# Performance work log

Hardware: AMD Instinct MI355X
Metric: run time of the kernel (lower is better)

The kernel has to match this reference:

```python
import jax, jax.numpy as jnp
import numpy as np


def _conv(x, w, stride, dil):
    # VALID conv in NCHW / OIHW layout with rhs (kernel) dilation
    return jax.lax.conv_general_dilated(
        x, w, window_strides=stride, padding='VALID', rhs_dilation=dil,
        dimension_numbers=('NCHW', 'OIHW', 'NCHW'))


def setup_inputs() -> dict:
    key = jax.random.key(0)
    k1, k2, k3 = jax.random.split(key, 3)
    B, Cin, H, W = 8, 64, 256, 256  # W even => columns_mod2 == 0
    Cout = 128
    inp = jax.random.normal(k1, (B, Cin, H, W), dtype=jnp.float32)
    # kaiming-normal-style init as in the torch module
    fan0 = Cin * 3 * 1
    kernel0 = jax.random.normal(k2, (Cout, Cin, 3, 1), dtype=jnp.float32) * np.float32(np.sqrt(2.0 / fan0))
    fan1 = Cin * 2 * 2
    kernel1 = jax.random.normal(k3, (Cout, Cin, 2, 2), dtype=jnp.float32) * np.float32(np.sqrt(2.0 / fan1))
    bias = jnp.full((Cout,), 0.01, dtype=jnp.float32)
    return {'input': inp, 'kernel0': kernel0, 'kernel1': kernel1, 'bias': bias}


def reference(input, kernel0, kernel1, bias):
    # hexagdly conv2d, size=1, stride=1, even number of columns (columns_mod2 = 0)
    x = input
    # kernel0: vertical 3x1 stencil over all columns; bias added once here
    even_all = _conv(jnp.pad(x, ((0, 0), (0, 0), (1, 1), (0, 0))), kernel0, (1, 1), (1, 1))
    even_all = even_all + bias[None, :, None, None]
    # kernel1: 2x2 stencil with horizontal dilation 2, stride 2 in width,
    # with column-parity-dependent vertical offset (hex grid)
    # odd columns: ZeroPad2d(left=1, right=0, top=1, bottom=0)
    ooc = _conv(jnp.pad(x, ((0, 0), (0, 0), (1, 0), (1, 0))), kernel1, (1, 2), (1, 2))
    # even columns: ZeroPad2d(left=0, right=1, top=0, bottom=1)
    oec = _conv(jnp.pad(x, ((0, 0), (0, 0), (0, 1), (0, 1))), kernel1, (1, 2), (1, 2))
    # interleave columns: out[..., 2k] = ooc[..., k], out[..., 2k+1] = oec[..., k]
    B, C, H, Wh = ooc.shape
    inter = jnp.stack([ooc, oec], axis=-1).reshape(B, C, H, 2 * Wh)
    return even_all + inter
```

## Files before the change

kernel.cpp:

```cpp
#include <hip/hip_runtime.h>
#include <hip/hip_bf16.h>


#define CIN  64
#define COUT 128
#define HH   256
#define WW   256
#define TH   8
#define TW   32
#define XR   10
#define XC   34

typedef __attribute__((ext_vector_type(8))) short short8;
typedef __attribute__((ext_vector_type(4))) float f32x4;

static __device__ __forceinline__ unsigned short f2bf(float v) {
    __hip_bfloat16 h = __float2bfloat16(v);
    return __builtin_bit_cast(unsigned short, h);
}

typedef __attribute__((address_space(1))) const unsigned int asg_u32;
typedef __attribute__((address_space(3))) unsigned int asl_u32;
static __device__ __forceinline__ void gl2lds16(const void* g, void* l) {
    __builtin_amdgcn_global_load_lds((asg_u32*)g, (asl_u32*)l, 16, 0, 0);
}

#define XS_BYTES   (XR * XC * CIN * 2)
#define WTB_OFF    XS_BYTES
#define SMEM_BYTES (XS_BYTES + 2 * COUT * CIN * 2)
#define OT_STRIDE  33
#define WTAP       (COUT * CIN)

__global__ __launch_bounds__(512)
void prep_weights(const float* __restrict__ k0, const float* __restrict__ k1,
                  unsigned short* __restrict__ wsw)
{
    const int idx = blockIdx.x * 512 + threadIdx.x;
    if (idx >= 7 * COUT * 8) return;
    const int t   = idx >> 10;
    const int co  = (idx >> 3) & 127;
    const int ci0 = (idx & 7) * 8;
    short8 wv;
    #pragma unroll
    for (int j = 0; j < 8; ++j) {
        const int ci = ci0 + j;
        float v = (t < 3) ? k0[(co * CIN + ci) * 3 + t]
                          : k1[(co * CIN + ci) * 4 + (t - 3)];
        wv[j] = (short)f2bf(v);
    }
    const int e = (co * CIN + ci0) ^ ((co & 7) * 8);
    *(short8*)&wsw[t * WTAP + e] = wv;
}

__global__ __launch_bounds__(512, 4)
void hexconv_mfma(const float* __restrict__ x,
                  const unsigned short* __restrict__ wsw,
                  const float* __restrict__ bias,
                  float* __restrict__ out)
{
    __shared__ alignas(16) char smem[SMEM_BYTES];
    __shared__ float bias_lds[COUT];
    unsigned short* xs  = (unsigned short*)smem;
    unsigned short* wtb = (unsigned short*)(smem + WTB_OFF);
    float*          ot  = (float*)smem;

    const int tid  = threadIdx.x;
    const int lane = tid & 63;
    const int wid  = tid >> 6;

    const int wg = (blockIdx.x & 7) * 256 + (blockIdx.x >> 3);
    const int bx = wg & 7;
    const int by = (wg >> 3) & 31;
    const int b  = wg >> 8;

    const int h0 = by * TH;
    const int w0 = bx * TW;

    auto stage_tap = [&](int t, int buf) {
        const unsigned short* s0 = wsw + t * WTAP + wid * 1024;
        unsigned short* d0 = wtb + buf * WTAP + wid * 1024;
        gl2lds16(s0 + lane * 8, d0);
        gl2lds16(s0 + 512 + lane * 8, d0 + 512);
    };

    stage_tap(0, 0);

    if (tid < COUT) bias_lds[tid] = bias[tid];

    {
        const float* xb = x + (size_t)b * CIN * HH * WW;
        const int c = tid & 31;
        const int g = tid >> 5;
        for (int p = g; p < XR * 32; p += 16) {
            const int cip = p & 31;
            const int row = p >> 5;
            const int ci  = cip * 2;
            const int gh  = h0 - 1 + row;
            float v0 = 0.f, v1 = 0.f;
            if ((unsigned)gh < HH) {
                const float* pr = xb + ((size_t)ci * HH + gh) * WW + w0 + c;
                v0 = pr[0];
                v1 = pr[HH * WW];
            }
            unsigned int pk = (unsigned int)f2bf(v0) | ((unsigned int)f2bf(v1) << 16);
            const int col = c + 1;
            const int e = ((row * XC + col) * CIN + ci) ^ ((col & 7) * 8);
            *(unsigned int*)&xs[e] = pk;
        }
        for (int i = tid; i < 2 * XR * CIN; i += 512) {
            const int side = (i >= XR * CIN) ? 1 : 0;
            const int rem  = i - side * XR * CIN;
            const int row  = rem >> 6;
            const int ci   = rem & 63;
            const int col  = side ? (XC - 1) : 0;
            const int gh   = h0 - 1 + row;
            const int gw   = side ? (w0 + TW) : (w0 - 1);
            float v = 0.f;
            if ((unsigned)gh < HH && (unsigned)gw < WW)
                v = xb[((size_t)ci * HH + gh) * WW + gw];
            const int e = ((row * XC + col) * CIN + ci) ^ ((col & 7) * 8);
            xs[e] = f2bf(v);
        }
    }

    __syncthreads();

    const int wm   = wid & 1;
    const int wn   = wid >> 1;
    const int c15  = lane & 15;
    const int q8   = (lane >> 4) * 8;
    const int par  = lane & 1;

    const int aBase = (wm * 64 + c15) * CIN + q8;
    const int swzA  = (c15 & 7) * 8;

    f32x4 acc[4][4];
    #pragma unroll
    for (int mi = 0; mi < 4; ++mi)
        #pragma unroll
        for (int ni = 0; ni < 4; ++ni)
            acc[mi][ni] = (f32x4)0.0f;

    for (int tap = 0; tap < 7; ++tap) {
        if (tap < 6) stage_tap(tap + 1, (tap + 1) & 1);

        const unsigned short* wc = wtb + (tap & 1) * WTAP;

        int R0, P, C0;
        if (tap < 3) { R0 = tap; P = 0; C0 = 1; }
        else { R0 = (tap - 3) >> 1; P = 1; C0 = ((tap - 3) & 1) * 2; }
        const int colb  = c15 + C0;
        const int swzB  = (colb & 7) * 8;
        const int bBase = ((wn * 2 + R0 + P * par) * XC + colb) * CIN + q8;

        #pragma unroll
        for (int ci0 = 0; ci0 < CIN; ci0 += 32) {
            short8 af[4];
            #pragma unroll
            for (int mi = 0; mi < 4; ++mi)
                af[mi] = *(const short8*)&wc[(aBase + mi * 16 * CIN + ci0) ^ swzA];
            #pragma unroll
            for (int ni = 0; ni < 4; ++ni) {
                const int hr = ni >> 1, chalf = ni & 1;
                const int e = (bBase + hr * (XC * CIN) + chalf * (16 * CIN) + ci0) ^ swzB;
                short8 bf = *(const short8*)&xs[e];
                #pragma unroll
                for (int mi = 0; mi < 4; ++mi)
                    acc[mi][ni] = __builtin_amdgcn_mfma_f32_16x16x32_bf16(
                        af[mi], bf, acc[mi][ni], 0, 0, 0);
            }
        }
        __syncthreads();
    }

    #pragma unroll
    for (int p = 0; p < 2; ++p) {
        if (wm == p) {
            #pragma unroll
            for (int mi = 0; mi < 4; ++mi) {
                #pragma unroll
                for (int ni = 0; ni < 4; ++ni) {
                    const int hh   = wn * 2 + (ni >> 1);
                    const int wloc = (ni & 1) * 16 + c15;
                    #pragma unroll
                    for (int r = 0; r < 4; ++r) {
                        const int col = mi * 16 + (lane >> 4) * 4 + r;
                        ot[(col * TH + hh) * OT_STRIDE + wloc] =
                            acc[mi][ni][r] + bias_lds[p * 64 + col];
                    }
                }
            }
        }
        __syncthreads();
        #pragma unroll
        for (int it = 0; it < 8; ++it) {
            const int col = it * 8 + (tid >> 6);
            const int hh  = (tid >> 3) & 7;
            const int w4  = (tid & 7) * 4;
            const float* src = &ot[(col * TH + hh) * OT_STRIDE + w4];
            f32x4 v = { src[0], src[1], src[2], src[3] };
            __builtin_nontemporal_store(v,
                (f32x4*)&out[(((size_t)b * COUT + p * 64 + col) * HH + h0 + hh) * WW + w0 + w4]);
        }
        if (p == 0) __syncthreads();
    }
}

extern "C" void kernel_launch(void* const* d_in, const int* in_sizes, int n_in,
                              void* d_out, int out_size, void* d_ws, size_t ws_size,
                              hipStream_t stream) {
    const float* x    = (const float*)d_in[0];
    const float* k0   = (const float*)d_in[1];
    const float* k1   = (const float*)d_in[2];
    const float* bias = (const float*)d_in[3];
    float* out        = (float*)d_out;
    unsigned short* wsw = (unsigned short*)d_ws;

    prep_weights<<<dim3(14, 1, 1), 512, 0, stream>>>(k0, k1, wsw);
    hexconv_mfma<<<dim3(2048, 1, 1), 512, 0, stream>>>(x, wsw, bias, out);
}
```

Baseline: 113.7 us.

## Vectorize input tile loads and replace syncthreads with fine-grained waitcnt barriers

The input tile staging now loads four consecutive floats per thread with 128-bit global loads instead of scalar loads, which cuts the number of load instructions. The tap loop is fully unrolled, and each __syncthreads is replaced by explicit s_waitcnt vmcnt/lgkmcnt plus raw s_barrier. This lets the next tap's weight prefetch stay in flight while the current tap computes, instead of draining every outstanding memory operation at each barrier. The vmcnt(2) counting assumes that only the two prefetch loads are outstanding. If the compiler reorders or adds loads, this could cause a subtle race.

Result: faster. 98.41 us (-13.4%).

```diff
diff --git a/kernel.cpp b/kernel.cpp
--- a/kernel.cpp
+++ b/kernel.cpp
@@ -89,23 +89,27 @@
 
     {
         const float* xb = x + (size_t)b * CIN * HH * WW;
-        const int c = tid & 31;
-        const int g = tid >> 5;
-        for (int p = g; p < XR * 32; p += 16) {
-            const int cip = p & 31;
-            const int row = p >> 5;
-            const int ci  = cip * 2;
+        const int cg = tid & 7;
+        const int u0 = tid >> 3;
+        #pragma unroll
+        for (int it = 0; it < 5; ++it) {
+            const int u   = u0 + it * 64;
+            const int row = u >> 5;
+            const int ci  = (u & 31) * 2;
             const int gh  = h0 - 1 + row;
-            float v0 = 0.f, v1 = 0.f;
+            f32x4 a = (f32x4)0.0f, c = (f32x4)0.0f;
             if ((unsigned)gh < HH) {
-                const float* pr = xb + ((size_t)ci * HH + gh) * WW + w0 + c;
-                v0 = pr[0];
-                v1 = pr[HH * WW];
-            }
-            unsigned int pk = (unsigned int)f2bf(v0) | ((unsigned int)f2bf(v1) << 16);
-            const int col = c + 1;
-            const int e = ((row * XC + col) * CIN + ci) ^ ((col & 7) * 8);
-            *(unsigned int*)&xs[e] = pk;
+                const float* pb = xb + ((size_t)ci * HH + gh) * WW + w0 + 4 * cg;
+                a = *(const f32x4*)pb;
+                c = *(const f32x4*)(pb + HH * WW);
+            }
+            #pragma unroll
+            for (int k = 0; k < 4; ++k) {
+                const int col = 4 * cg + 1 + k;
+                unsigned int pk = (unsigned int)f2bf(a[k]) | ((unsigned int)f2bf(c[k]) << 16);
+                const int e = ((row * XC + col) * CIN + ci) ^ ((col & 7) * 8);
+                *(unsigned int*)&xs[e] = pk;
+            }
         }
         for (int i = tid; i < 2 * XR * CIN; i += 512) {
             const int side = (i >= XR * CIN) ? 1 : 0;
@@ -141,8 +145,16 @@
         for (int ni = 0; ni < 4; ++ni)
             acc[mi][ni] = (f32x4)0.0f;
 
+    #pragma unroll
     for (int tap = 0; tap < 7; ++tap) {
-        if (tap < 6) stage_tap(tap + 1, (tap + 1) & 1);
+        if (tap < 6) {
+            stage_tap(tap + 1, (tap + 1) & 1);
+            asm volatile("s_waitcnt vmcnt(2)" ::: "memory");
+        } else {
+            asm volatile("s_waitcnt vmcnt(0)" ::: "memory");
+        }
+        __builtin_amdgcn_s_barrier();
+        __builtin_amdgcn_sched_barrier(0);
 
         const unsigned short* wc = wtb + (tap & 1) * WTAP;
 
@@ -170,7 +182,10 @@
                         af[mi], bf, acc[mi][ni], 0, 0, 0);
             }
         }
-        __syncthreads();
+
+        asm volatile("s_waitcnt lgkmcnt(0)" ::: "memory");
+        __builtin_amdgcn_sched_barrier(0);
+        __builtin_amdgcn_s_barrier();
     }
 
     #pragma unroll
@@ -191,7 +206,9 @@
                 }
             }
         }
-        __syncthreads();
+        asm volatile("s_waitcnt lgkmcnt(0)" ::: "memory");
+        __builtin_amdgcn_sched_barrier(0);
+        __builtin_amdgcn_s_barrier();
         #pragma unroll
         for (int it = 0; it < 8; ++it) {
             const int col = it * 8 + (tid >> 6);
@@ -202,7 +219,11 @@
             __builtin_nontemporal_store(v,
                 (f32x4*)&out[(((size_t)b * COUT + p * 64 + col) * HH + h0 + hh) * WW + w0 + w4]);
         }
-        if (p == 0) __syncthreads();
+        if (p == 0) {
+            asm volatile("s_waitcnt lgkmcnt(0)" ::: "memory");
+            __builtin_amdgcn_sched_barrier(0);
+            __builtin_amdgcn_s_barrier();
+        }
     }
 }
 
```
